# Performance work log

Hardware: AMD Instinct MI355X
Metric: run time of the kernel (lower is better)

The kernel has to match this reference:

```python
import jax, jax.numpy as jnp
import numpy as np

N_NODES = 100000
N_EDGES = 1600000
IN_F = 128
OUT_F = 64
ORDER = 3


def setup_inputs() -> dict:
    key = jax.random.key(0)
    k1, k2, k3, k4, k5 = jax.random.split(key, 5)
    x = jax.random.normal(k1, (N_NODES, IN_F), dtype=jnp.float32)
    edge_index = jax.random.randint(k2, (2, N_EDGES), 0, N_NODES, dtype=jnp.int64)
    edge_weight = jax.random.uniform(k3, (N_EDGES,), dtype=jnp.float32)
    # nn.Linear default init scale ~ 1/sqrt(in_features)
    W_weight = jax.random.normal(k4, (OUT_F, IN_F), dtype=jnp.float32) / np.sqrt(IN_F)
    W_bias = jax.random.normal(k5, (OUT_F,), dtype=jnp.float32) / np.sqrt(IN_F)
    return {"x": x, "edge_index": edge_index, "edge_weight": edge_weight,
            "W_weight": W_weight, "W_bias": W_bias}


def _spmm(edge_index, edge_weight, h):
    # out[dst] = sum_e edge_weight[e] * h[src[e]]
    src, dst = edge_index[0], edge_index[1]
    msg = edge_weight[:, None] * h[src]          # [E, OUT_F] gathered messages
    return jax.ops.segment_sum(msg, dst, num_segments=N_NODES)


def reference(x, edge_index, edge_weight, W_weight, W_bias):
    # Linear projection: [N, IN_F] -> [N, OUT_F]
    h = x @ W_weight.T + W_bias
    # `order` hops of sparse propagation
    for _ in range(ORDER):
        h = _spmm(edge_index, edge_weight, h)
    return h
```

## Files before the change

kernel.cpp:

```cpp
#include <hip/hip_runtime.h>
#include <hip/hip_fp16.h>

#define N_NODES_C 100000
#define N_EDGES_C 1600000
#define IN_F 128
#define OUT_F 64

#define BIN_SHIFT 9
#define BIN_SZ    512
#define NBIN      ((N_NODES_C + BIN_SZ - 1) / BIN_SZ)
#define NCHUNK    256
#define CH        (N_EDGES_C / NCHUNK)

__global__ __launch_bounds__(256) void gemm_kernel(
    const float* __restrict__ x, const float* __restrict__ W,
    const float* __restrict__ bias, __half* __restrict__ h, int n) {
  __shared__ float Wt[IN_F * OUT_F];
  const int t = threadIdx.x;
  {
    const int o = t & 63;
    const int k4base = t >> 6;
    const float4* Wrow = (const float4*)(W + o * IN_F);
#pragma unroll
    for (int i = 0; i < 8; ++i) {
      int k4 = k4base + i * 4;
      float4 v = Wrow[k4];
      int k = k4 * 4;
      Wt[(k + 0) * OUT_F + o] = v.x;
      Wt[(k + 1) * OUT_F + o] = v.y;
      Wt[(k + 2) * OUT_F + o] = v.z;
      Wt[(k + 3) * OUT_F + o] = v.w;
    }
  }
  __syncthreads();

  const int tx = t & 15;
  const int ty = t >> 4;
  const int node0 = blockIdx.x * 64 + ty * 4;

  bool v0 = node0 + 0 < n, v1 = node0 + 1 < n, v2 = node0 + 2 < n, v3 = node0 + 3 < n;
  const float4* xr0 = (const float4*)(x + (size_t)(v0 ? node0 + 0 : 0) * IN_F);
  const float4* xr1 = (const float4*)(x + (size_t)(v1 ? node0 + 1 : 0) * IN_F);
  const float4* xr2 = (const float4*)(x + (size_t)(v2 ? node0 + 2 : 0) * IN_F);
  const float4* xr3 = (const float4*)(x + (size_t)(v3 ? node0 + 3 : 0) * IN_F);

  float4 acc0 = make_float4(0.f, 0.f, 0.f, 0.f);
  float4 acc1 = acc0, acc2 = acc0, acc3 = acc0;
  const float4* Wt4 = (const float4*)Wt;

#pragma unroll 2
  for (int kc = 0; kc < 32; ++kc) {
    float4 xv0 = xr0[kc];
    float4 xv1 = xr1[kc];
    float4 xv2 = xr2[kc];
    float4 xv3 = xr3[kc];
    float4 w0 = Wt4[(kc * 4 + 0) * 16 + tx];
    float4 w1 = Wt4[(kc * 4 + 1) * 16 + tx];
    float4 w2 = Wt4[(kc * 4 + 2) * 16 + tx];
    float4 w3 = Wt4[(kc * 4 + 3) * 16 + tx];
#define FMA4(A, XV)                                            \
    A.x += XV.x * w0.x + XV.y * w1.x + XV.z * w2.x + XV.w * w3.x; \
    A.y += XV.x * w0.y + XV.y * w1.y + XV.z * w2.y + XV.w * w3.y; \
    A.z += XV.x * w0.z + XV.y * w1.z + XV.z * w2.z + XV.w * w3.z; \
    A.w += XV.x * w0.w + XV.y * w1.w + XV.z * w2.w + XV.w * w3.w;
    FMA4(acc0, xv0)
    FMA4(acc1, xv1)
    FMA4(acc2, xv2)
    FMA4(acc3, xv3)
#undef FMA4
  }

  const float4 bv = ((const float4*)bias)[tx];
  acc0.x += bv.x; acc0.y += bv.y; acc0.z += bv.z; acc0.w += bv.w;
  acc1.x += bv.x; acc1.y += bv.y; acc1.z += bv.z; acc1.w += bv.w;
  acc2.x += bv.x; acc2.y += bv.y; acc2.z += bv.z; acc2.w += bv.w;
  acc3.x += bv.x; acc3.y += bv.y; acc3.z += bv.z; acc3.w += bv.w;

#define STORE16(A, NODE, VALID)                                         \
  if (VALID) {                                                          \
    union { __half2 h2[2]; uint2 u; } pk;                               \
    pk.h2[0] = __floats2half2_rn(A.x, A.y);                             \
    pk.h2[1] = __floats2half2_rn(A.z, A.w);                             \
    ((uint2*)((char*)h + (size_t)(NODE) * 128))[tx] = pk.u;             \
  }
  STORE16(acc0, node0 + 0, v0)
  STORE16(acc1, node0 + 1, v1)
  STORE16(acc2, node0 + 2, v2)
  STORE16(acc3, node0 + 3, v3)
#undef STORE16
}

__global__ __launch_bounds__(256) void hist_kernel(
    const int* __restrict__ dst, int* __restrict__ hist) {
  __shared__ int h[NBIN];
  const int t = threadIdx.x;
  for (int i = t; i < NBIN; i += 256) h[i] = 0;
  __syncthreads();
  const int e0 = blockIdx.x * CH;
  for (int i = t; i < CH; i += 256)
    atomicAdd(&h[dst[e0 + i] >> BIN_SHIFT], 1);
  __syncthreads();
  for (int i = t; i < NBIN; i += 256)
    hist[i * NCHUNK + blockIdx.x] = h[i];
}

#define RB 256
__global__ __launch_bounds__(RB) void reduce_kernel(
    const int* __restrict__ v, int* __restrict__ blockSums, int n) {
  __shared__ int s[RB];
  int i = blockIdx.x * RB + threadIdx.x;
  s[threadIdx.x] = (i < n) ? v[i] : 0;
  __syncthreads();
  for (int off = RB / 2; off > 0; off >>= 1) {
    if (threadIdx.x < off) s[threadIdx.x] += s[threadIdx.x + off];
    __syncthreads();
  }
  if (threadIdx.x == 0) blockSums[blockIdx.x] = s[0];
}

__global__ __launch_bounds__(512) void scan_partials_kernel(
    const int* __restrict__ blockSums, int* __restrict__ blockOffs, int nb,
    int* __restrict__ total_out) {
  __shared__ int s[512];
  int t = threadIdx.x;
  int v = (t < nb) ? blockSums[t] : 0;
  s[t] = v;
  __syncthreads();
  for (int off = 1; off < 512; off <<= 1) {
    int u = (t >= off) ? s[t - off] : 0;
    __syncthreads();
    s[t] += u;
    __syncthreads();
  }
  if (t < nb) blockOffs[t] = s[t] - v;
  if (t == 511) *total_out = s[511];
}

__global__ __launch_bounds__(RB) void scan_final_kernel(
    const int* __restrict__ hist, const int* __restrict__ blockOffs,
    int* __restrict__ soff, int* __restrict__ binStart, int n) {
  __shared__ int s[RB];
  int i = blockIdx.x * RB + threadIdx.x;
  int v = (i < n) ? hist[i] : 0;
  s[threadIdx.x] = v;
  __syncthreads();
  for (int off = 1; off < RB; off <<= 1) {
    int u = (threadIdx.x >= off) ? s[threadIdx.x - off] : 0;
    __syncthreads();
    s[threadIdx.x] += u;
    __syncthreads();
  }
  if (i < n) {
    int ex = blockOffs[blockIdx.x] + s[threadIdx.x] - v;
    soff[i] = ex;
    if (threadIdx.x == 0) binStart[blockIdx.x] = ex;
  }
}

__global__ __launch_bounds__(256) void binscatter_kernel(
    const int* __restrict__ src, const int* __restrict__ dst,
    const float* __restrict__ w, const int* __restrict__ soff,
    int* __restrict__ stage_d, int2* __restrict__ stage_sw) {
  __shared__ int lcur[NBIN];
  const int t = threadIdx.x;
  const int c = blockIdx.x;
  for (int i = t; i < NBIN; i += 256) lcur[i] = soff[i * NCHUNK + c];
  __syncthreads();
  const int e0 = c * CH;
  for (int i = t; i < CH; i += 256) {
    int e = e0 + i;
    int d = dst[e];
    int p = atomicAdd(&lcur[d >> BIN_SHIFT], 1);
    stage_d[p]  = d;
    stage_sw[p] = make_int2(src[e] * OUT_F, __float_as_int(w[e]));
  }
}

__global__ __launch_bounds__(BIN_SZ) void place_kernel(
    const int* __restrict__ binStart, const int* __restrict__ stage_d,
    const int2* __restrict__ stage_sw, int* __restrict__ row_ptr,
    int2* __restrict__ edges, int n) {
  __shared__ int lcount[BIN_SZ];
  __shared__ int s[BIN_SZ];
  __shared__ int lcur[BIN_SZ];
  const int t = threadIdx.x;
  const int b = blockIdx.x;
  const int base = binStart[b];
  const int end  = (b == NBIN - 1) ? N_EDGES_C : binStart[b + 1];
  const int node0 = b << BIN_SHIFT;

  lcount[t] = 0;
  __syncthreads();
  for (int i = base + t; i < end; i += BIN_SZ)
    atomicAdd(&lcount[stage_d[i] - node0], 1);
  __syncthreads();

  int v = lcount[t];
  s[t] = v;
  __syncthreads();
  for (int off = 1; off < BIN_SZ; off <<= 1) {
    int u = (t >= off) ? s[t - off] : 0;
    __syncthreads();
    s[t] += u;
    __syncthreads();
  }
  int ex = base + s[t] - v;
  int node = node0 + t;
  if (node < n) row_ptr[node] = ex;
  lcur[t] = ex;
  __syncthreads();

  for (int i = base + t; i < end; i += BIN_SZ) {
    int d = stage_d[i];
    int p = atomicAdd(&lcur[d - node0], 1);
    edges[p] = stage_sw[i];
  }
  if (b == NBIN - 1 && t == 0) row_ptr[n] = N_EDGES_C;
}

__device__ inline void fma8_h(float* acc, uint4 r, float w) {
  unsigned u[4] = {r.x, r.y, r.z, r.w};
#pragma unroll
  for (int q = 0; q < 4; ++q) {
    __half2 h2 = *reinterpret_cast<__half2*>(&u[q]);
    float2 f = __half22float2(h2);
    acc[2 * q + 0] += w * f.x;
    acc[2 * q + 1] += w * f.y;
  }
}

template <int OUT32>
__global__ __launch_bounds__(256) void spmm16_kernel(
    const int* __restrict__ row_ptr, const int2* __restrict__ edges,
    const __half* __restrict__ hin, void* __restrict__ hout, int n) {
  const int node = blockIdx.x * 32 + (threadIdx.x >> 3);
  const int fl   = threadIdx.x & 7;
  if (node >= n) return;
  const int beg = row_ptr[node];
  const int end = row_ptr[node + 1];

  float acc[8] = {0.f, 0.f, 0.f, 0.f, 0.f, 0.f, 0.f, 0.f};
  int j = beg;
  for (; j + 3 < end; j += 4) {
    int2 e0 = edges[j + 0];
    int2 e1 = edges[j + 1];
    int2 e2 = edges[j + 2];
    int2 e3 = edges[j + 3];
    uint4 r0 = ((const uint4*)(hin + e0.x))[fl];
    uint4 r1 = ((const uint4*)(hin + e1.x))[fl];
    uint4 r2 = ((const uint4*)(hin + e2.x))[fl];
    uint4 r3 = ((const uint4*)(hin + e3.x))[fl];
    fma8_h(acc, r0, __int_as_float(e0.y));
    fma8_h(acc, r1, __int_as_float(e1.y));
    fma8_h(acc, r2, __int_as_float(e2.y));
    fma8_h(acc, r3, __int_as_float(e3.y));
  }
  for (; j < end; ++j) {
    int2 e = edges[j];
    uint4 r = ((const uint4*)(hin + e.x))[fl];
    fma8_h(acc, r, __int_as_float(e.y));
  }

  if (OUT32) {
    float* op = (float*)hout + (size_t)node * OUT_F + 8 * fl;
    ((float4*)op)[0] = make_float4(acc[0], acc[1], acc[2], acc[3]);
    ((float4*)op)[1] = make_float4(acc[4], acc[5], acc[6], acc[7]);
  } else {
    union { __half2 h2[4]; uint4 u; } pk;
#pragma unroll
    for (int q = 0; q < 4; ++q)
      pk.h2[q] = __floats2half2_rn(acc[2 * q], acc[2 * q + 1]);
    ((uint4*)((char*)hout + (size_t)node * 128))[fl] = pk.u;
  }
}

extern "C" void kernel_launch(void* const* d_in, const int* in_sizes, int n_in,
                              void* d_out, int out_size, void* d_ws, size_t ws_size,
                              hipStream_t stream) {
  const float* x    = (const float*)d_in[0];
  const int*   ei   = (const int*)d_in[1];
  const float* ew   = (const float*)d_in[2];
  const float* W    = (const float*)d_in[3];
  const float* bias = (const float*)d_in[4];
  float* out = (float*)d_out;

  const int N = N_NODES_C;
  const int E = N_EDGES_C;
  const int* src = ei;
  const int* dst = ei + E;
  const int NH = NBIN * NCHUNK;
  const int NRB = NH / RB;

  char* p = (char*)d_ws;
  auto carve = [&](size_t bytes) {
    void* r = (void*)p;
    p += (bytes + 255) & ~(size_t)255;
    return r;
  };
  __half* h16A     = (__half*)carve((size_t)N * OUT_F * 2);
  __half* h16B     = (__half*)carve((size_t)N * OUT_F * 2);
  int*   row_ptr   = (int*)  carve((size_t)(N + 1) * 4);
  int2*  edges     = (int2*) carve((size_t)E * 8);
  int*   hist      = (int*)  carve((size_t)NH * 4);
  int*   soff      = (int*)  carve((size_t)NH * 4);
  int*   blockSums = (int*)  carve((size_t)NRB * 4);
  int*   blockOffs = (int*)  carve((size_t)NRB * 4);
  int*   binStart  = (int*)  carve((size_t)(NBIN + 1) * 4);

  int2* stage_sw = (int2*)d_out;
  int*  stage_d  = (int*)((char*)d_out + (size_t)E * 8);

  hist_kernel         <<<NCHUNK, 256, 0, stream>>>(dst, hist);
  reduce_kernel       <<<NRB, RB, 0, stream>>>(hist, blockSums, NH);
  scan_partials_kernel<<<1, 512, 0, stream>>>(blockSums, blockOffs, NRB, &binStart[NBIN]);
  scan_final_kernel   <<<NRB, RB, 0, stream>>>(hist, blockOffs, soff, binStart, NH);
  binscatter_kernel   <<<NCHUNK, 256, 0, stream>>>(src, dst, ew, soff, stage_d, stage_sw);
  place_kernel        <<<NBIN, BIN_SZ, 0, stream>>>(binStart, stage_d, stage_sw,
                                                    row_ptr, edges, N);

  gemm_kernel<<<(N + 63) / 64, 256, 0, stream>>>(x, W, bias, h16A, N);

  spmm16_kernel<0><<<(N + 31) / 32, 256, 0, stream>>>(row_ptr, edges, h16A, h16B, N);
  spmm16_kernel<0><<<(N + 31) / 32, 256, 0, stream>>>(row_ptr, edges, h16B, h16A, N);
  spmm16_kernel<1><<<(N + 31) / 32, 256, 0, stream>>>(row_ptr, edges, h16A, out, N);
}
```

Baseline: 303.6 us.

## Replace scalar FP32 projection GEMM with FP16 MFMA matrix-core kernel

Rewrites the linear projection so each wavefront computes a 16-node by 64-output tile using 16x16x32 fp16 MFMA instructions. Weights are loaded directly into register fragments and converted to fp16, which removes the LDS transpose and the scalar FMA loop. The inputs x and W are now rounded to fp16 before multiplication, so the projection loses some precision. Output stores are scalar half writes with a strided pattern, and the kernel assumes N is a multiple of 16.

```diff
diff --git a/kernel.cpp b/kernel.cpp
--- a/kernel.cpp
+++ b/kernel.cpp
@@ -12,82 +12,67 @@
 #define NCHUNK    256
 #define CH        (N_EDGES_C / NCHUNK)
 
-__global__ __launch_bounds__(256) void gemm_kernel(
+typedef __attribute__((ext_vector_type(8))) _Float16 half8;
+typedef __attribute__((ext_vector_type(4))) float    f32x4;
+
+__global__ __launch_bounds__(256) void gemm_mfma_kernel(
     const float* __restrict__ x, const float* __restrict__ W,
-    const float* __restrict__ bias, __half* __restrict__ h, int n) {
-  __shared__ float Wt[IN_F * OUT_F];
-  const int t = threadIdx.x;
-  {
-    const int o = t & 63;
-    const int k4base = t >> 6;
-    const float4* Wrow = (const float4*)(W + o * IN_F);
-#pragma unroll
-    for (int i = 0; i < 8; ++i) {
-      int k4 = k4base + i * 4;
-      float4 v = Wrow[k4];
-      int k = k4 * 4;
-      Wt[(k + 0) * OUT_F + o] = v.x;
-      Wt[(k + 1) * OUT_F + o] = v.y;
-      Wt[(k + 2) * OUT_F + o] = v.z;
-      Wt[(k + 3) * OUT_F + o] = v.w;
+    const float* __restrict__ bias, _Float16* __restrict__ h, int n) {
+  const int wid  = threadIdx.x >> 6;
+  const int lane = threadIdx.x & 63;
+  const int lr   = lane & 15;
+  const int lg   = lane >> 4;
+
+  const int tile = blockIdx.x * 4 + wid;
+  if (tile * 16 >= n) return;
+  const int node0 = tile * 16;
+
+  half8 bfrag[4][4];
+#pragma unroll
+  for (int nc = 0; nc < 4; ++nc) {
+    const float* wrow = W + (size_t)(nc * 16 + lr) * IN_F + lg * 8;
+#pragma unroll
+    for (int kc = 0; kc < 4; ++kc) {
+      float4 a = ((const float4*)(wrow + kc * 32))[0];
+      float4 b = ((const float4*)(wrow + kc * 32))[1];
+      half8 f;
+      f[0] = (_Float16)a.x; f[1] = (_Float16)a.y;
+      f[2] = (_Float16)a.z; f[3] = (_Float16)a.w;
+      f[4] = (_Float16)b.x; f[5] = (_Float16)b.y;
+      f[6] = (_Float16)b.z; f[7] = (_Float16)b.w;
+      bfrag[nc][kc] = f;
     }
   }
-  __syncthreads();
-
-  const int tx = t & 15;
-  const int ty = t >> 4;
-  const int node0 = blockIdx.x * 64 + ty * 4;
-
-  bool v0 = node0 + 0 < n, v1 = node0 + 1 < n, v2 = node0 + 2 < n, v3 = node0 + 3 < n;
-  const float4* xr0 = (const float4*)(x + (size_t)(v0 ? node0 + 0 : 0) * IN_F);
-  const float4* xr1 = (const float4*)(x + (size_t)(v1 ? node0 + 1 : 0) * IN_F);
-  const float4* xr2 = (const float4*)(x + (size_t)(v2 ? node0 + 2 : 0) * IN_F);
-  const float4* xr3 = (const float4*)(x + (size_t)(v3 ? node0 + 3 : 0) * IN_F);
-
-  float4 acc0 = make_float4(0.f, 0.f, 0.f, 0.f);
-  float4 acc1 = acc0, acc2 = acc0, acc3 = acc0;
-  const float4* Wt4 = (const float4*)Wt;
-
-#pragma unroll 2
-  for (int kc = 0; kc < 32; ++kc) {
-    float4 xv0 = xr0[kc];
-    float4 xv1 = xr1[kc];
-    float4 xv2 = xr2[kc];
-    float4 xv3 = xr3[kc];
-    float4 w0 = Wt4[(kc * 4 + 0) * 16 + tx];
-    float4 w1 = Wt4[(kc * 4 + 1) * 16 + tx];
-    float4 w2 = Wt4[(kc * 4 + 2) * 16 + tx];
-    float4 w3 = Wt4[(kc * 4 + 3) * 16 + tx];
-#define FMA4(A, XV)                                            \
-    A.x += XV.x * w0.x + XV.y * w1.x + XV.z * w2.x + XV.w * w3.x; \
-    A.y += XV.x * w0.y + XV.y * w1.y + XV.z * w2.y + XV.w * w3.y; \
-    A.z += XV.x * w0.z + XV.y * w1.z + XV.z * w2.z + XV.w * w3.z; \
-    A.w += XV.x * w0.w + XV.y * w1.w + XV.z * w2.w + XV.w * w3.w;
-    FMA4(acc0, xv0)
-    FMA4(acc1, xv1)
-    FMA4(acc2, xv2)
-    FMA4(acc3, xv3)
-#undef FMA4
-  }
-
-  const float4 bv = ((const float4*)bias)[tx];
-  acc0.x += bv.x; acc0.y += bv.y; acc0.z += bv.z; acc0.w += bv.w;
-  acc1.x += bv.x; acc1.y += bv.y; acc1.z += bv.z; acc1.w += bv.w;
-  acc2.x += bv.x; acc2.y += bv.y; acc2.z += bv.z; acc2.w += bv.w;
-  acc3.x += bv.x; acc3.y += bv.y; acc3.z += bv.z; acc3.w += bv.w;
-
-#define STORE16(A, NODE, VALID)                                         \
-  if (VALID) {                                                          \
-    union { __half2 h2[2]; uint2 u; } pk;                               \
-    pk.h2[0] = __floats2half2_rn(A.x, A.y);                             \
-    pk.h2[1] = __floats2half2_rn(A.z, A.w);                             \
-    ((uint2*)((char*)h + (size_t)(NODE) * 128))[tx] = pk.u;             \
-  }
-  STORE16(acc0, node0 + 0, v0)
-  STORE16(acc1, node0 + 1, v1)
-  STORE16(acc2, node0 + 2, v2)
-  STORE16(acc3, node0 + 3, v3)
-#undef STORE16
+
+  float bv[4];
+#pragma unroll
+  for (int nc = 0; nc < 4; ++nc) bv[nc] = bias[nc * 16 + lr];
+
+  const float* xp = x + (size_t)(node0 + lr) * IN_F + lg * 8;
+  f32x4 acc[4] = {{0.f, 0.f, 0.f, 0.f}, {0.f, 0.f, 0.f, 0.f},
+                  {0.f, 0.f, 0.f, 0.f}, {0.f, 0.f, 0.f, 0.f}};
+#pragma unroll
+  for (int kc = 0; kc < 4; ++kc) {
+    float4 a = ((const float4*)(xp + kc * 32))[0];
+    float4 b = ((const float4*)(xp + kc * 32))[1];
+    half8 af;
+    af[0] = (_Float16)a.x; af[1] = (_Float16)a.y;
+    af[2] = (_Float16)a.z; af[3] = (_Float16)a.w;
+    af[4] = (_Float16)b.x; af[5] = (_Float16)b.y;
+    af[6] = (_Float16)b.z; af[7] = (_Float16)b.w;
+#pragma unroll
+    for (int nc = 0; nc < 4; ++nc)
+      acc[nc] = __builtin_amdgcn_mfma_f32_16x16x32_f16(af, bfrag[nc][kc], acc[nc], 0, 0, 0);
+  }
+
+#pragma unroll
+  for (int nc = 0; nc < 4; ++nc) {
+#pragma unroll
+    for (int r = 0; r < 4; ++r) {
+      int node = node0 + lg * 4 + r;
+      h[(size_t)node * OUT_F + nc * 16 + lr] = (_Float16)(acc[nc][r] + bv[nc]);
+    }
+  }
 }
 
 __global__ __launch_bounds__(256) void hist_kernel(
@@ -318,7 +303,7 @@
   place_kernel        <<<NBIN, BIN_SZ, 0, stream>>>(binStart, stage_d, stage_sw,
                                                     row_ptr, edges, N);
 
-  gemm_kernel<<<(N + 63) / 64, 256, 0, stream>>>(x, W, bias, h16A, N);
+  gemm_mfma_kernel<<<(N / 16 + 3) / 4, 256, 0, stream>>>(x, W, bias, (_Float16*)h16A, N);
 
   spmm16_kernel<0><<<(N + 31) / 32, 256, 0, stream>>>(row_ptr, edges, h16A, h16B, N);
   spmm16_kernel<0><<<(N + 31) / 32, 256, 0, stream>>>(row_ptr, edges, h16B, h16A, N);
```

Measured after the change: 279.7 us. -7.9%, faster.
